# Performance work log

Hardware: AMD Instinct MI355X
Metric: run time of the kernel (lower is better)

## Reference

```python
import jax, jax.numpy as jnp
import numpy as np

B, S, D = 1, 4096, 2048
M = 4                  # compression rate
NC = S // M            # compressed slots
TOPK = 512
NH, C = 16, 64         # query heads, head dim
DC = 512               # query compression dim
NG, DG = 4, 512        # output projection groups, intermediate dim
CI, NHI = 64, 4        # indexer head dim, indexer heads
ROPE = 32              # partial rope dims (last ROPE of C)
EPS = 1e-6
NEG = -1e30


def _ln(x, w, b):
    mu = x.mean(-1, keepdims=True)
    var = ((x - mu) ** 2).mean(-1, keepdims=True)
    return (x - mu) * jax.lax.rsqrt(var + EPS) * w + b


def _rope(q, pos):
    # partial RoPE on the last ROPE dims of q [B,S,NH,C]; keys are NOT rotated (faithful)
    x_part, x_rope = q[..., :C - ROPE], q[..., C - ROPE:]
    x0, x1 = x_rope[..., 0::2], x_rope[..., 1::2]
    inv = 1.0 / (10000.0 ** (jnp.arange(0, ROPE, 2, dtype=jnp.float32) / ROPE))
    ang = pos[:, None].astype(jnp.float32) * inv[None]           # [S, ROPE/2]
    cos = jnp.cos(ang)[None, :, None, :]
    sin = jnp.sin(ang)[None, :, None, :]
    r = x0 * cos - x1 * sin
    i = x0 * sin + x1 * cos
    rot = jnp.stack([r, i], -1).reshape(x_rope.shape)
    return jnp.concatenate([x_part, rot], -1)


def reference(x, w_kv_a, w_kv_b, w_z_a, w_z_b, b_a, b_b, w_dq, w_iuq, w_w, w_k,
              w_uq, o_down, o_up, kvn_w, kvn_b, qn_w, qn_b, sink_logits):
    pos = jnp.arange(S)
    # ---- token-level compressor: windowed (2m-wide, m-stride) per-channel softmax ----
    c_a = (x @ w_kv_a).reshape(B, NC, M, C)
    c_b = (x @ w_kv_b).reshape(B, NC, M, C)
    z_a = (x @ w_z_a).reshape(B, NC, M, C)
    z_b = (x @ w_z_b).reshape(B, NC, M, C)
    prev_z = jnp.concatenate([jnp.full((B, 1, M, C), NEG, x.dtype), z_b[:, :-1]], 1)
    prev_c = jnp.concatenate([jnp.zeros((B, 1, M, C), x.dtype), c_b[:, :-1]], 1)
    logits = jnp.concatenate([prev_z + b_b, z_a + b_a], 2)        # [B,NC,2M,C]
    wts = jax.nn.softmax(logits, axis=2)
    compressed = (wts * jnp.concatenate([prev_c, c_a], 2)).sum(2)  # [B,NC,C]
    # ---- lightning indexer: relu multi-head scores + causal mask + top-k ----
    c_q = x @ w_dq                                                 # [B,S,DC]
    q_i = (c_q @ w_iuq).reshape(B, S, NHI, CI)
    hw = x @ w_w                                                   # [B,S,NHI]
    k_orig = x.reshape(B, NC, M, D).mean(2)
    k_proj = k_orig @ w_k                                          # [B,NC,CI]
    dot = jnp.einsum('bshc,bkc->bskh', q_i, k_proj)
    iscores = (jax.nn.relu(dot) * hw[:, :, None, :]).sum(-1)       # [B,S,NC]
    imask = jnp.arange(NC)[None, None, :] < pos[None, :, None]     # NC//S + 1 == 1
    iscores = jnp.where(imask, iscores, -jnp.inf)
    _, top_idx = jax.lax.top_k(iscores, TOPK)                      # [B,S,K]
    # ---- sparse attention over gathered compressed KV ----
    q = (c_q @ w_uq).reshape(B, S, NH, C)
    kc = _ln(compressed, kvn_w, kvn_b)
    q = _rope(_ln(q, qn_w, qn_b), pos)
    k_sel = kc[jnp.arange(B)[:, None, None], top_idx]              # [B,S,K,C]
    scores = jnp.einsum('bshc,bskc->bhsk', q, k_sel) / jnp.sqrt(jnp.float32(C))
    cmask = pos[None, None, :, None] < (top_idx[:, None, :, :] * M)
    scores = jnp.where(cmask, scores, -jnp.inf)
    e = jnp.exp(scores)
    denom = e.sum(-1, keepdims=True) + jnp.exp(sink_logits)[None, :, None, None]
    attn = e / denom                                               # sink-augmented softmax
    out = jnp.einsum('bhsk,bskc->bshc', attn, k_sel).reshape(B, S, NH * C)
    g = jnp.einsum('bsgd,gde->bsge', out.reshape(B, S, NG, (NH * C) // NG), o_down)
    return g.reshape(B, S, NG * DG) @ o_up


def setup_inputs() -> dict:
    key = jax.random.key(0)
    ks = jax.random.split(key, 20)
    lin = lambda k, fi, fo: jax.random.normal(k, (fi, fo), jnp.float32) / np.sqrt(fi)
    return {
        'x': jax.random.normal(ks[0], (B, S, D), jnp.float32),
        'w_kv_a': lin(ks[1], D, C), 'w_kv_b': lin(ks[2], D, C),
        'w_z_a': lin(ks[3], D, C), 'w_z_b': lin(ks[4], D, C),
        'b_a': 0.02 * jax.random.normal(ks[5], (M, C), jnp.float32),
        'b_b': 0.02 * jax.random.normal(ks[6], (M, C), jnp.float32),
        'w_dq': lin(ks[7], D, DC),
        'w_iuq': lin(ks[8], DC, CI * NHI),
        'w_w': lin(ks[9], D, NHI),
        'w_k': lin(ks[10], D, CI),
        'w_uq': lin(ks[11], DC, NH * C),
        'o_down': jax.random.normal(ks[12], (NG, (NH * C) // NG, DG), jnp.float32) / np.sqrt((NH * C) // NG),
        'o_up': lin(ks[13], NG * DG, D),
        'kvn_w': 1.0 + 0.02 * jax.random.normal(ks[14], (C,), jnp.float32),
        'kvn_b': 0.02 * jax.random.normal(ks[15], (C,), jnp.float32),
        'qn_w': 1.0 + 0.02 * jax.random.normal(ks[16], (C,), jnp.float32),
        'qn_b': 0.02 * jax.random.normal(ks[17], (C,), jnp.float32),
        'sink_logits': 0.02 * jax.random.normal(ks[18], (NH,), jnp.float32),
    }
```

## Files before the change

### kernel.cpp

```cpp
#include <hip/hip_runtime.h>
#include <math.h>

#define S_   4096
#define D_   2048
#define M_   4
#define NC_  1024
#define TOPK_ 512
#define NH_  16
#define C_   64
#define DC_  512
#define NG_  4
#define DG_  512
#define CI_  64
#define NHI_ 4
#define ROPE_ 32
#define EPS_ 1e-6f

typedef __attribute__((ext_vector_type(8))) short short8;
typedef __attribute__((ext_vector_type(4))) short short4v;
typedef __attribute__((ext_vector_type(4))) float floatx4;

__device__ inline unsigned short f2bf(float f) {
  unsigned u = __float_as_uint(f);
  u += 0x7fff + ((u >> 16) & 1);
  return (unsigned short)(u >> 16);
}
__device__ inline float bf2f(unsigned short h) {
  return __uint_as_float(((unsigned)h) << 16);
}

#define GLD16(src, dst) __builtin_amdgcn_global_load_lds( \
    (const __attribute__((address_space(1))) unsigned int*)(src), \
    (__attribute__((address_space(3))) unsigned int*)(dst), 16, 0, 0)

__device__ inline void xcd_remap(int& bx, int& by, int& bz) {
  int nx = gridDim.x, ny = gridDim.y;
  int flat = blockIdx.x + nx * (blockIdx.y + ny * blockIdx.z);
  int nwg = nx * ny * (int)gridDim.z;
  int swz = (flat & 7) * (nwg >> 3) + (flat >> 3);
  bx = swz % nx;
  int t = swz / nx;
  by = t % ny;
  bz = t / ny;
}

__global__ __launch_bounds__(256) void gemm_bf16_64(
    const unsigned short* __restrict__ A, const unsigned short* __restrict__ Bt,
    float* __restrict__ Cf, unsigned short* __restrict__ Cb,
    int K, int lda, int ldb, int ldc,
    long long Az, long long Bz, long long Cz) {
  int bx, by, zz;
  xcd_remap(bx, by, zz);
  A += (size_t)zz * Az;
  Bt += (size_t)zz * Bz;
  if (Cf) Cf += (size_t)zz * Cz;
  if (Cb) Cb += (size_t)zz * Cz;
  __shared__ unsigned short As[2 * 2 * 64 * 32];
  __shared__ unsigned short Bs[2 * 2 * 128 * 32];
  int tid = threadIdx.x;
  int bm = by * 64, bn = bx * 128;
  int lane = tid & 63, wid = tid >> 6;
  int wm = (wid & 1) * 32, wn = (wid >> 1) * 64;
  int qd = lane >> 4, m16 = lane & 15;

  floatx4 acc[2][4];
#pragma unroll
  for (int i = 0; i < 2; ++i)
#pragma unroll
    for (int j = 0; j < 4; ++j) acc[i][j] = (floatx4){0.f, 0.f, 0.f, 0.f};

  auto stage = [&](int buf, int kt) {
#pragma unroll
    for (int h = 0; h < 2; ++h) {
      {
        int rr = tid >> 2, ss = tid & 3;
        int gg = ss ^ ((rr >> 1) & 3);
        GLD16(A + (size_t)(bm + rr) * lda + kt + h * 32 + gg * 8,
              &As[(buf * 2 + h) * 2048 + tid * 8]);
      }
#pragma unroll
      for (int i = 0; i < 2; ++i) {
        int idx = tid + 256 * i;
        int rr = idx >> 2, ss = idx & 3;
        int gg = ss ^ ((rr >> 1) & 3);
        GLD16(Bt + (size_t)(bn + rr) * ldb + kt + h * 32 + gg * 8,
              &Bs[(buf * 2 + h) * 4096 + idx * 8]);
      }
    }
  };
  auto compute = [&](int buf) {
#pragma unroll
    for (int h = 0; h < 2; ++h) {
      const unsigned short* Ab = &As[(buf * 2 + h) * 2048];
      const unsigned short* Bb = &Bs[(buf * 2 + h) * 4096];
      short8 af[2], bfr[4];
#pragma unroll
      for (int mi = 0; mi < 2; ++mi) {
        int r = wm + mi * 16 + m16;
        int slot = qd ^ ((r >> 1) & 3);
        af[mi] = *(const short8*)&Ab[r * 32 + slot * 8];
      }
#pragma unroll
      for (int ni = 0; ni < 4; ++ni) {
        int r = wn + ni * 16 + m16;
        int slot = qd ^ ((r >> 1) & 3);
        bfr[ni] = *(const short8*)&Bb[r * 32 + slot * 8];
      }
#pragma unroll
      for (int mi = 0; mi < 2; ++mi)
#pragma unroll
        for (int ni = 0; ni < 4; ++ni)
          acc[mi][ni] = __builtin_amdgcn_mfma_f32_16x16x32_bf16(af[mi], bfr[ni], acc[mi][ni], 0, 0, 0);
    }
  };

  stage(0, 0);
  __syncthreads();
  int cur = 0;
  for (int kt = 64; kt < K; kt += 64) {
    stage(cur ^ 1, kt);
    compute(cur);
    __syncthreads();
    cur ^= 1;
  }
  compute(cur);

#pragma unroll
  for (int mi = 0; mi < 2; ++mi)
#pragma unroll
    for (int ni = 0; ni < 4; ++ni) {
      int col = bn + wn + ni * 16 + m16;
#pragma unroll
      for (int rg = 0; rg < 4; ++rg) {
        int row = bm + wm + mi * 16 + qd * 4 + rg;
        if (Cb)
          Cb[(size_t)row * ldc + col] = f2bf(acc[mi][ni][rg]);
        else
          Cf[(size_t)row * ldc + col] = acc[mi][ni][rg];
      }
    }
}

__global__ __launch_bounds__(256) void gemm_bf16_128(
    const unsigned short* __restrict__ A, const unsigned short* __restrict__ Bt,
    float* __restrict__ Cf, unsigned short* __restrict__ Cb,
    int K, int lda, int ldb, int ldc,
    long long Az, long long Bz, long long Cz) {
  int zz = blockIdx.z;
  A += (size_t)zz * Az;
  Bt += (size_t)zz * Bz;
  if (Cf) Cf += (size_t)zz * Cz;
  if (Cb) Cb += (size_t)zz * Cz;
  __shared__ unsigned short As[2 * 2 * 128 * 32];
  __shared__ unsigned short Bs[2 * 2 * 128 * 32];
  int tid = threadIdx.x;
  int bm = blockIdx.y * 128, bn = blockIdx.x * 128;
  int lane = tid & 63, wid = tid >> 6;
  int wm = (wid & 1) * 64, wn = (wid >> 1) * 64;
  int qd = lane >> 4, m16 = lane & 15;

  floatx4 acc[4][4];
#pragma unroll
  for (int i = 0; i < 4; ++i)
#pragma unroll
    for (int j = 0; j < 4; ++j) acc[i][j] = (floatx4){0.f, 0.f, 0.f, 0.f};

  auto stage = [&](int buf, int kt) {
#pragma unroll
    for (int h = 0; h < 2; ++h) {
#pragma unroll
      for (int i = 0; i < 2; ++i) {
        int idx = tid + 256 * i;
        int rr = idx >> 2, ss = idx & 3;
        int gg = ss ^ ((rr >> 1) & 3);
        GLD16(A + (size_t)(bm + rr) * lda + kt + h * 32 + gg * 8,
              &As[(buf * 2 + h) * 4096 + idx * 8]);
        GLD16(Bt + (size_t)(bn + rr) * ldb + kt + h * 32 + gg * 8,
              &Bs[(buf * 2 + h) * 4096 + idx * 8]);
      }
    }
  };
  auto compute = [&](int buf) {
#pragma unroll
    for (int h = 0; h < 2; ++h) {
      const unsigned short* Ab = &As[(buf * 2 + h) * 4096];
      const unsigned short* Bb = &Bs[(buf * 2 + h) * 4096];
      short8 af[4], bfr[4];
#pragma unroll
      for (int mi = 0; mi < 4; ++mi) {
        int r = wm + mi * 16 + m16;
        int slot = qd ^ ((r >> 1) & 3);
        af[mi] = *(const short8*)&Ab[r * 32 + slot * 8];
      }
#pragma unroll
      for (int ni = 0; ni < 4; ++ni) {
        int r = wn + ni * 16 + m16;
        int slot = qd ^ ((r >> 1) & 3);
        bfr[ni] = *(const short8*)&Bb[r * 32 + slot * 8];
      }
#pragma unroll
      for (int mi = 0; mi < 4; ++mi)
#pragma unroll
        for (int ni = 0; ni < 4; ++ni)
          acc[mi][ni] = __builtin_amdgcn_mfma_f32_16x16x32_bf16(af[mi], bfr[ni], acc[mi][ni], 0, 0, 0);
    }
  };

  stage(0, 0);
  __syncthreads();
  int cur = 0;
  for (int kt = 64; kt < K; kt += 64) {
    stage(cur ^ 1, kt);
    compute(cur);
    __syncthreads();
    cur ^= 1;
  }
  compute(cur);

#pragma unroll
  for (int mi = 0; mi < 4; ++mi)
#pragma unroll
    for (int ni = 0; ni < 4; ++ni) {
      int col = bn + wn + ni * 16 + m16;
#pragma unroll
      for (int rg = 0; rg < 4; ++rg) {
        int row = bm + wm + mi * 16 + qd * 4 + rg;
        if (Cb)
          Cb[(size_t)row * ldc + col] = f2bf(acc[mi][ni][rg]);
        else
          Cf[(size_t)row * ldc + col] = acc[mi][ni][rg];
      }
    }
}

__global__ __launch_bounds__(256) void gemm_bf16_split_64(
    const unsigned short* __restrict__ Ah, const unsigned short* __restrict__ Al,
    const unsigned short* __restrict__ Bh, const unsigned short* __restrict__ Bl,
    float* __restrict__ Cf, int K, int lda, int ldb, int ldc,
    long long Az, long long Bz, long long Cz) {
  int bx, by, zz;
  xcd_remap(bx, by, zz);
  Ah += (size_t)zz * Az; Al += (size_t)zz * Az;
  Bh += (size_t)zz * Bz; Bl += (size_t)zz * Bz;
  Cf += (size_t)zz * Cz;
  __shared__ unsigned short Ash[64 * 32];
  __shared__ unsigned short Asl[64 * 32];
  __shared__ unsigned short Bsh[128 * 32];
  __shared__ unsigned short Bsl[128 * 32];
  int tid = threadIdx.x;
  int bm = by * 64, bn = bx * 128;
  int lane = tid & 63, wid = tid >> 6;
  int wm = (wid & 1) * 32, wn = (wid >> 1) * 64;
  int qd = lane >> 4, m16 = lane & 15;

  floatx4 acc[2][4];
#pragma unroll
  for (int i = 0; i < 2; ++i)
#pragma unroll
    for (int j = 0; j < 4; ++j) acc[i][j] = (floatx4){0.f, 0.f, 0.f, 0.f};

  for (int k0 = 0; k0 < K; k0 += 32) {
    {
      int r = tid >> 2, sl = tid & 3;
      int g = sl ^ ((r >> 1) & 3);
      size_t aoff = (size_t)(bm + r) * lda + k0 + g * 8;
      GLD16(Ah + aoff, &Ash[tid * 8]);
      GLD16(Al + aoff, &Asl[tid * 8]);
    }
#pragma unroll
    for (int i = 0; i < 2; ++i) {
      int idx = tid + 256 * i;
      int r = idx >> 2, sl = idx & 3;
      int g = sl ^ ((r >> 1) & 3);
      size_t boff = (size_t)(bn + r) * ldb + k0 + g * 8;
      GLD16(Bh + boff, &Bsh[idx * 8]);
      GLD16(Bl + boff, &Bsl[idx * 8]);
    }
    __syncthreads();
    short8 afh[2], afl[2], bfh[4], bfl[4];
#pragma unroll
    for (int mi = 0; mi < 2; ++mi) {
      int r = wm + mi * 16 + m16;
      int slot = qd ^ ((r >> 1) & 3);
      afh[mi] = *(const short8*)&Ash[r * 32 + slot * 8];
      afl[mi] = *(const short8*)&Asl[r * 32 + slot * 8];
    }
#pragma unroll
    for (int ni = 0; ni < 4; ++ni) {
      int r = wn + ni * 16 + m16;
      int slot = qd ^ ((r >> 1) & 3);
      bfh[ni] = *(const short8*)&Bsh[r * 32 + slot * 8];
      bfl[ni] = *(const short8*)&Bsl[r * 32 + slot * 8];
    }
#pragma unroll
    for (int mi = 0; mi < 2; ++mi)
#pragma unroll
      for (int ni = 0; ni < 4; ++ni) {
        acc[mi][ni] = __builtin_amdgcn_mfma_f32_16x16x32_bf16(afh[mi], bfh[ni], acc[mi][ni], 0, 0, 0);
        acc[mi][ni] = __builtin_amdgcn_mfma_f32_16x16x32_bf16(afh[mi], bfl[ni], acc[mi][ni], 0, 0, 0);
        acc[mi][ni] = __builtin_amdgcn_mfma_f32_16x16x32_bf16(afl[mi], bfh[ni], acc[mi][ni], 0, 0, 0);
      }
    __syncthreads();
  }
#pragma unroll
  for (int mi = 0; mi < 2; ++mi)
#pragma unroll
    for (int ni = 0; ni < 4; ++ni) {
      int col = bn + wn + ni * 16 + m16;
#pragma unroll
      for (int rg = 0; rg < 4; ++rg) {
        int row = bm + wm + mi * 16 + qd * 4 + rg;
        Cf[(size_t)row * ldc + col] = acc[mi][ni][rg];
      }
    }
}

__global__ __launch_bounds__(256) void gemm_bf16_split_128(
    const unsigned short* __restrict__ Ah, const unsigned short* __restrict__ Al,
    const unsigned short* __restrict__ Bh, const unsigned short* __restrict__ Bl,
    float* __restrict__ Cf, int K, int lda, int ldb, int ldc,
    long long Az, long long Bz, long long Cz) {
  int bx, by, zz;
  xcd_remap(bx, by, zz);
  Ah += (size_t)zz * Az; Al += (size_t)zz * Az;
  Bh += (size_t)zz * Bz; Bl += (size_t)zz * Bz;
  Cf += (size_t)zz * Cz;
  __shared__ unsigned short Ash[2 * 128 * 32];
  __shared__ unsigned short Asl[2 * 128 * 32];
  __shared__ unsigned short Bsh[2 * 128 * 32];
  __shared__ unsigned short Bsl[2 * 128 * 32];
  int tid = threadIdx.x;
  int bm = by * 128, bn = bx * 128;
  int lane = tid & 63, wid = tid >> 6;
  int wm = (wid & 1) * 64, wn = (wid >> 1) * 64;
  int qd = lane >> 4, m16 = lane & 15;

  floatx4 acc[4][4];
#pragma unroll
  for (int i = 0; i < 4; ++i)
#pragma unroll
    for (int j = 0; j < 4; ++j) acc[i][j] = (floatx4){0.f, 0.f, 0.f, 0.f};

  auto stage = [&](int buf, int kt) {
#pragma unroll
    for (int i = 0; i < 2; ++i) {
      int idx = tid + 256 * i;
      int rr = idx >> 2, ss = idx & 3;
      int gg = ss ^ ((rr >> 1) & 3);
      size_t aoff = (size_t)(bm + rr) * lda + kt + gg * 8;
      size_t boff = (size_t)(bn + rr) * ldb + kt + gg * 8;
      GLD16(Ah + aoff, &Ash[buf * 4096 + idx * 8]);
      GLD16(Al + aoff, &Asl[buf * 4096 + idx * 8]);
      GLD16(Bh + boff, &Bsh[buf * 4096 + idx * 8]);
      GLD16(Bl + boff, &Bsl[buf * 4096 + idx * 8]);
    }
  };
  auto compute = [&](int buf) {
    const unsigned short* Ahb = &Ash[buf * 4096];
    const unsigned short* Alb = &Asl[buf * 4096];
    const unsigned short* Bhb = &Bsh[buf * 4096];
    const unsigned short* Blb = &Bsl[buf * 4096];
    short8 afh[4], afl[4], bfh[4], bfl[4];
#pragma unroll
    for (int mi = 0; mi < 4; ++mi) {
      int r = wm + mi * 16 + m16;
      int slot = qd ^ ((r >> 1) & 3);
      afh[mi] = *(const short8*)&Ahb[r * 32 + slot * 8];
      afl[mi] = *(const short8*)&Alb[r * 32 + slot * 8];
    }
#pragma unroll
    for (int ni = 0; ni < 4; ++ni) {
      int r = wn + ni * 16 + m16;
      int slot = qd ^ ((r >> 1) & 3);
      bfh[ni] = *(const short8*)&Bhb[r * 32 + slot * 8];
      bfl[ni] = *(const short8*)&Blb[r * 32 + slot * 8];
    }
#pragma unroll
    for (int mi = 0; mi < 4; ++mi)
#pragma unroll
      for (int ni = 0; ni < 4; ++ni) {
        acc[mi][ni] = __builtin_amdgcn_mfma_f32_16x16x32_bf16(afh[mi], bfh[ni], acc[mi][ni], 0, 0, 0);
        acc[mi][ni] = __builtin_amdgcn_mfma_f32_16x16x32_bf16(afh[mi], bfl[ni], acc[mi][ni], 0, 0, 0);
        acc[mi][ni] = __builtin_amdgcn_mfma_f32_16x16x32_bf16(afl[mi], bfh[ni], acc[mi][ni], 0, 0, 0);
      }
  };

  stage(0, 0);
  __syncthreads();
  int cur = 0;
  for (int kt = 32; kt < K; kt += 32) {
    stage(cur ^ 1, kt);
    compute(cur);
    __syncthreads();
    cur ^= 1;
  }
  compute(cur);

#pragma unroll
  for (int mi = 0; mi < 4; ++mi)
#pragma unroll
    for (int ni = 0; ni < 4; ++ni) {
      int col = bn + wn + ni * 16 + m16;
#pragma unroll
      for (int rg = 0; rg < 4; ++rg) {
        int row = bm + wm + mi * 16 + qd * 4 + rg;
        Cf[(size_t)row * ldc + col] = acc[mi][ni][rg];
      }
    }
}

__global__ void reduce_f32(const float* __restrict__ P, float* __restrict__ C, int n, int z) {
  int i = (blockIdx.x * 256 + threadIdx.x) * 4;
  if (i >= n) return;
  float4 a = *(const float4*)&P[i];
  for (int s = 1; s < z; ++s) {
    float4 b = *(const float4*)&P[(size_t)s * n + i];
    a.x += b.x; a.y += b.y; a.z += b.z; a.w += b.w;
  }
  *(float4*)&C[i] = a;
}

__global__ void reduce_cast_split(const float* __restrict__ P, unsigned short* __restrict__ hi,
                                  unsigned short* __restrict__ lo, int n, int z) {
  int i = (blockIdx.x * 256 + threadIdx.x) * 4;
  if (i >= n) return;
  float4 a = *(const float4*)&P[i];
  for (int s = 1; s < z; ++s) {
    float4 b = *(const float4*)&P[(size_t)s * n + i];
    a.x += b.x; a.y += b.y; a.z += b.z; a.w += b.w;
  }
  ushort4 h = make_ushort4(f2bf(a.x), f2bf(a.y), f2bf(a.z), f2bf(a.w));
  ushort4 l = make_ushort4(f2bf(a.x - bf2f(h.x)), f2bf(a.y - bf2f(h.y)),
                           f2bf(a.z - bf2f(h.z)), f2bf(a.w - bf2f(h.w)));
  *(ushort4*)&hi[i] = h;
  *(ushort4*)&lo[i] = l;
}

__global__ __launch_bounds__(256) void iscores_mfma(
    const unsigned short* __restrict__ Ah, const unsigned short* __restrict__ Al,
    const unsigned short* __restrict__ Bh, const unsigned short* __restrict__ Bl,
    const float* __restrict__ hw, float* __restrict__ isc) {
  int bm = blockIdx.y * 128, bn = blockIdx.x * 128;
  if (bn > (bm >> 2) + 30) return;
  __shared__ unsigned short Ash[128 * 32];
  __shared__ unsigned short Asl[128 * 32];
  __shared__ unsigned short Bsh[128 * 32];
  __shared__ unsigned short Bsl[128 * 32];
  int tid = threadIdx.x;
  int lane = tid & 63, wid = tid >> 6;
  int wm = (wid >> 1) * 64, wn = (wid & 1) * 64;
  int qd = lane >> 4, m16 = lane & 15;

  floatx4 acc[4][4];
#pragma unroll
  for (int i = 0; i < 4; ++i)
#pragma unroll
    for (int j = 0; j < 4; ++j) acc[i][j] = (floatx4){0.f, 0.f, 0.f, 0.f};

#pragma unroll
  for (int k0 = 0; k0 < 64; k0 += 32) {
#pragma unroll
    for (int i = 0; i < 2; ++i) {
      int idx = tid + 256 * i;
      int r = idx >> 2, s = idx & 3;
      int g = s ^ ((r >> 1) & 3);
      size_t aoff = (size_t)(bm + r) * 64 + k0 + g * 8;
      size_t boff = (size_t)(bn + r) * 64 + k0 + g * 8;
      GLD16(Ah + aoff, &Ash[idx * 8]);
      GLD16(Al + aoff, &Asl[idx * 8]);
      GLD16(Bh + boff, &Bsh[idx * 8]);
      GLD16(Bl + boff, &Bsl[idx * 8]);
    }
    __syncthreads();
    short8 afh[4], afl[4], bfh[4], bfl[4];
#pragma unroll
    for (int mi = 0; mi < 4; ++mi) {
      int r = wm + mi * 16 + m16;
      int slot = qd ^ ((r >> 1) & 3);
      afh[mi] = *(const short8*)&Ash[r * 32 + slot * 8];
      afl[mi] = *(const short8*)&Asl[r * 32 + slot * 8];
    }
#pragma unroll
    for (int ni = 0; ni < 4; ++ni) {
      int r = wn + ni * 16 + m16;
      int slot = qd ^ ((r >> 1) & 3);
      bfh[ni] = *(const short8*)&Bsh[r * 32 + slot * 8];
      bfl[ni] = *(const short8*)&Bsl[r * 32 + slot * 8];
    }
#pragma unroll
    for (int mi = 0; mi < 4; ++mi)
#pragma unroll
      for (int ni = 0; ni < 4; ++ni) {
        acc[mi][ni] = __builtin_amdgcn_mfma_f32_16x16x32_bf16(afh[mi], bfh[ni], acc[mi][ni], 0, 0, 0);
        acc[mi][ni] = __builtin_amdgcn_mfma_f32_16x16x32_bf16(afh[mi], bfl[ni], acc[mi][ni], 0, 0, 0);
        acc[mi][ni] = __builtin_amdgcn_mfma_f32_16x16x32_bf16(afl[mi], bfh[ni], acc[mi][ni], 0, 0, 0);
      }
    __syncthreads();
  }
#pragma unroll
  for (int mi = 0; mi < 4; ++mi) {
    int tok = ((bm + wm + mi * 16) >> 2) + qd;
    float4 hwv = *(const float4*)&hw[tok * 4];
#pragma unroll
    for (int ni = 0; ni < 4; ++ni) {
      floatx4 a = acc[mi][ni];
      float v = fmaxf(a[0], 0.f) * hwv.x + fmaxf(a[1], 0.f) * hwv.y +
                fmaxf(a[2], 0.f) * hwv.z + fmaxf(a[3], 0.f) * hwv.w;
      int col = bn + wn + ni * 16 + m16;
      isc[(size_t)tok * NC_ + col] = (col < tok) ? v : -__builtin_inff();
    }
  }
}

#define BM 64
#define BN 64
#define BK 16
#define KSL_ 16
#define KSLICE_ 128
__global__ __launch_bounds__(256) void gemm_f32_splitk(
    const float* __restrict__ A, const float* __restrict__ B,
    float* __restrict__ P, int lda, int ldb) {
  __shared__ float As[BK][BM + 4];
  __shared__ float Bs[BK][BN + 4];
  int tid = threadIdx.x;
  int bm = blockIdx.y * BM;
  int kbase = blockIdx.x * KSLICE_;
  int tr = tid >> 4;
  int tc = tid & 15;
  float acc[4][4] = {{0.f}};
  for (int k0 = kbase; k0 < kbase + KSLICE_; k0 += BK) {
    int ac = tid & 15;
    int ar0 = tid >> 4;
#pragma unroll
    for (int i = 0; i < 4; ++i) {
      int r = ar0 + 16 * i;
      As[ac][r] = A[(size_t)(bm + r) * lda + k0 + ac];
    }
    int bc = tid & 63;
    int br0 = tid >> 6;
#pragma unroll
    for (int i = 0; i < 4; ++i) {
      int r = br0 + 4 * i;
      Bs[r][bc] = B[(size_t)(k0 + r) * ldb + bc];
    }
    __syncthreads();
#pragma unroll
    for (int kk = 0; kk < BK; ++kk) {
      float4 av = *(const float4*)&As[kk][tr * 4];
      float4 bv = *(const float4*)&Bs[kk][tc * 4];
      float a[4] = {av.x, av.y, av.z, av.w};
      float b[4] = {bv.x, bv.y, bv.z, bv.w};
#pragma unroll
      for (int i = 0; i < 4; ++i)
#pragma unroll
        for (int j = 0; j < 4; ++j) acc[i][j] += a[i] * b[j];
    }
    __syncthreads();
  }
  float* Pb = P + (size_t)blockIdx.x * (NC_ * CI_);
#pragma unroll
  for (int i = 0; i < 4; ++i) {
    float4 v = make_float4(acc[i][0], acc[i][1], acc[i][2], acc[i][3]);
    *(float4*)&Pb[(size_t)(bm + tr * 4 + i) * CI_ + tc * 4] = v;
  }
}

__global__ void reduce_splitk(const float* __restrict__ P, float* __restrict__ C) {
  int i = blockIdx.x * 256 + threadIdx.x;
  if (i >= NC_ * CI_) return;
  float a = 0.f;
#pragma unroll
  for (int s = 0; s < KSL_; ++s) a += P[(size_t)s * (NC_ * CI_) + i];
  C[i] = a;
}

__global__ void cast_bf16(const float* __restrict__ in, unsigned short* __restrict__ out, int n) {
  int i = (blockIdx.x * 256 + threadIdx.x) * 4;
  if (i >= n) return;
  float4 v = *(const float4*)&in[i];
  ushort4 o = make_ushort4(f2bf(v.x), f2bf(v.y), f2bf(v.z), f2bf(v.w));
  *(ushort4*)&out[i] = o;
}

__global__ void cast_split(const float* __restrict__ in, unsigned short* __restrict__ hi,
                           unsigned short* __restrict__ lo, int n) {
  int i = (blockIdx.x * 256 + threadIdx.x) * 4;
  if (i >= n) return;
  float4 v = *(const float4*)&in[i];
  ushort4 h = make_ushort4(f2bf(v.x), f2bf(v.y), f2bf(v.z), f2bf(v.w));
  ushort4 l = make_ushort4(f2bf(v.x - bf2f(h.x)), f2bf(v.y - bf2f(h.y)),
                           f2bf(v.z - bf2f(h.z)), f2bf(v.w - bf2f(h.w)));
  *(ushort4*)&hi[i] = h;
  *(ushort4*)&lo[i] = l;
}

__device__ inline float wave_sum64(float v) {
#pragma unroll
  for (int off = 32; off > 0; off >>= 1) v += __shfl_xor(v, off, 64);
  return v;
}

__global__ __launch_bounds__(512) void cast_split_hw_mean(
    const float* __restrict__ x, unsigned short* __restrict__ hi,
    unsigned short* __restrict__ lo, const float* __restrict__ ww,
    float* __restrict__ hw, float* __restrict__ ko) {
  int j = blockIdx.x, tid = threadIdx.x;
  int d0 = tid * 4;
  const float* wr = ww + d0 * 4;
  float4 v[4];
  float a[4][4];
#pragma unroll
  for (int m = 0; m < 4; ++m) {
    size_t i = (size_t)(j * 4 + m) * D_ + d0;
    v[m] = *(const float4*)&x[i];
    ushort4 h = make_ushort4(f2bf(v[m].x), f2bf(v[m].y), f2bf(v[m].z), f2bf(v[m].w));
    ushort4 l = make_ushort4(f2bf(v[m].x - bf2f(h.x)), f2bf(v[m].y - bf2f(h.y)),
                             f2bf(v[m].z - bf2f(h.z)), f2bf(v[m].w - bf2f(h.w)));
    *(ushort4*)&hi[i] = h;
    *(ushort4*)&lo[i] = l;
    a[m][0] = v[m].x * wr[0] + v[m].y * wr[4] + v[m].z * wr[8]  + v[m].w * wr[12];
    a[m][1] = v[m].x * wr[1] + v[m].y * wr[5] + v[m].z * wr[9]  + v[m].w * wr[13];
    a[m][2] = v[m].x * wr[2] + v[m].y * wr[6] + v[m].z * wr[10] + v[m].w * wr[14];
    a[m][3] = v[m].x * wr[3] + v[m].y * wr[7] + v[m].z * wr[11] + v[m].w * wr[15];
  }
  float4 s4;
  s4.x = 0.25f * (v[0].x + v[1].x + v[2].x + v[3].x);
  s4.y = 0.25f * (v[0].y + v[1].y + v[2].y + v[3].y);
  s4.z = 0.25f * (v[0].z + v[1].z + v[2].z + v[3].z);
  s4.w = 0.25f * (v[0].w + v[1].w + v[2].w + v[3].w);
  *(float4*)&ko[(size_t)j * D_ + d0] = s4;
#pragma unroll
  for (int m = 0; m < 4; ++m)
#pragma unroll
    for (int h2 = 0; h2 < 4; ++h2) a[m][h2] = wave_sum64(a[m][h2]);
  __shared__ float red[8][16];
  int wid = tid >> 6, lane = tid & 63;
  if (lane == 0) {
#pragma unroll
    for (int m = 0; m < 4; ++m)
#pragma unroll
      for (int h2 = 0; h2 < 4; ++h2) red[wid][m * 4 + h2] = a[m][h2];
  }
  __syncthreads();
  if (tid < 16) {
    float acc = 0.f;
#pragma unroll
    for (int w2 = 0; w2 < 8; ++w2) acc += red[w2][tid];
    hw[(size_t)(j * 4 + (tid >> 2)) * 4 + (tid & 3)] = acc;
  }
}

__global__ __launch_bounds__(256) void transpose_cast(
    const float* __restrict__ in, unsigned short* __restrict__ out, int K, int N,
    long long inz, long long outz) {
  in += (size_t)blockIdx.z * inz;
  out += (size_t)blockIdx.z * outz;
  __shared__ float t[32][33];
  int k0 = blockIdx.x * 32, n0 = blockIdx.y * 32;
  int tx = threadIdx.x & 31, ty = threadIdx.x >> 5;
#pragma unroll
  for (int i = 0; i < 4; ++i)
    t[ty * 4 + i][tx] = in[(size_t)(k0 + ty * 4 + i) * N + n0 + tx];
  __syncthreads();
#pragma unroll
  for (int i = 0; i < 4; ++i)
    out[(size_t)(n0 + ty * 4 + i) * K + k0 + tx] = f2bf(t[tx][ty * 4 + i]);
}

__global__ __launch_bounds__(256) void transpose_cast_split(
    const float* __restrict__ in, unsigned short* __restrict__ outh,
    unsigned short* __restrict__ outl, int K, int N) {
  __shared__ float t[32][33];
  int k0 = blockIdx.x * 32, n0 = blockIdx.y * 32;
  int tx = threadIdx.x & 31, ty = threadIdx.x >> 5;
#pragma unroll
  for (int i = 0; i < 4; ++i)
    t[ty * 4 + i][tx] = in[(size_t)(k0 + ty * 4 + i) * N + n0 + tx];
  __syncthreads();
#pragma unroll
  for (int i = 0; i < 4; ++i) {
    float v = t[tx][ty * 4 + i];
    unsigned short h = f2bf(v);
    outh[(size_t)(n0 + ty * 4 + i) * K + k0 + tx] = h;
    outl[(size_t)(n0 + ty * 4 + i) * K + k0 + tx] = f2bf(v - bf2f(h));
  }
}

__global__ void gate_kernel(const float* __restrict__ c4,
                            const float* __restrict__ ba, const float* __restrict__ bb,
                            float* __restrict__ comp) {
  int i = blockIdx.x * 256 + threadIdx.x;
  if (i >= NC_ * C_) return;
  int j = i >> 6, c = i & 63;
  float lg[8], vv[8];
#pragma unroll
  for (int m = 0; m < 4; ++m) {
    if (j == 0) {
      lg[m] = -1e30f + bb[m * C_ + c];
      vv[m] = 0.f;
    } else {
      int row = (j - 1) * 4 + m;
      lg[m] = c4[(size_t)row * 256 + 192 + c] + bb[m * C_ + c];
      vv[m] = c4[(size_t)row * 256 + 64 + c];
    }
    int row2 = j * 4 + m;
    lg[4 + m] = c4[(size_t)row2 * 256 + 128 + c] + ba[m * C_ + c];
    vv[4 + m] = c4[(size_t)row2 * 256 + 0 + c];
  }
  float mx = lg[0];
#pragma unroll
  for (int t = 1; t < 8; ++t) mx = fmaxf(mx, lg[t]);
  float se = 0.f, acc = 0.f;
#pragma unroll
  for (int t = 0; t < 8; ++t) {
    float e = expf(lg[t] - mx);
    se += e;
    acc += e * vv[t];
  }
  comp[i] = acc / se;
}

__global__ void ln_kc_kernel(const float* __restrict__ in, const float* __restrict__ w,
                             const float* __restrict__ b, unsigned short* __restrict__ kcb,
                             unsigned short* __restrict__ kcbT) {
  int row = blockIdx.x * 4 + (threadIdx.x >> 6);
  int c = threadIdx.x & 63;
  float v = in[(size_t)row * C_ + c];
  float mu = wave_sum64(v) * (1.f / 64.f);
  float d = v - mu;
  float var = wave_sum64(d * d) * (1.f / 64.f);
  float y = d * (1.f / sqrtf(var + EPS_)) * w[c] + b[c];
  unsigned short h = f2bf(y);
  kcb[(size_t)row * C_ + c] = h;
  kcbT[(size_t)c * NC_ + row] = h;
}

__global__ void ln_rope_q_kernel(const float* __restrict__ quq, const float* __restrict__ w,
                                 const float* __restrict__ b, unsigned short* __restrict__ qb) {
  int row = blockIdx.x * 4 + (threadIdx.x >> 6);
  int s = row >> 4;
  int c = threadIdx.x & 63;
  float v = quq[(size_t)row * C_ + c];
  float mu = wave_sum64(v) * (1.f / 64.f);
  float d = v - mu;
  float var = wave_sum64(d * d) * (1.f / 64.f);
  float y = d * (1.f / sqrtf(var + EPS_)) * w[c] + b[c];
  float outv;
  float partner = __shfl_xor(y, 1, 64);
  if (c < C_ - ROPE_) {
    outv = y;
  } else {
    int p = (c - (C_ - ROPE_)) >> 1;
    float inv = powf(10000.f, -(2.f * (float)p) / (float)ROPE_);
    float ang = (float)s * inv;
    float cs = cosf(ang), sn = sinf(ang);
    if ((c & 1) == 0)
      outv = y * cs - partner * sn;
    else
      outv = partner * sn + y * cs;
  }
  qb[(size_t)row * C_ + c] = f2bf(outv * 0.125f);
}

#define MINF_ 0x007FFFFFu
__global__ __launch_bounds__(256) void topk_select_kernel(
    const float* __restrict__ isc, unsigned* __restrict__ sel) {
  __shared__ unsigned mv[NC_];
  __shared__ unsigned bins[256];
  __shared__ unsigned wsum[4];
  __shared__ unsigned sB, sR;
  __shared__ unsigned selw[32];
  int s = blockIdx.x;
  int tid = threadIdx.x;
  int w = tid >> 6, lane = tid & 63;
  if (tid < 32) selw[tid] = 0u;
  for (int i = tid; i < NC_; i += 256) {
    if (i < s) {
      unsigned u = __float_as_uint(isc[(size_t)s * NC_ + i]);
      mv[i] = (u & 0x80000000u) ? ~u : (u | 0x80000000u);
    } else {
      mv[i] = MINF_;
    }
  }
  __syncthreads();
  unsigned K_rem = TOPK_;
  unsigned prefix = 0u;
  for (int lvl = 0; lvl < 4; ++lvl) {
    int shift = 24 - 8 * lvl;
    unsigned pm = (lvl == 0) ? 0u : (0xFFFFFFFFu << (32 - 8 * lvl));
    bins[tid] = 0u;
    __syncthreads();
    for (int i = tid; i < NC_; i += 256) {
      unsigned m = mv[i];
      if ((m & pm) == prefix) atomicAdd(&bins[(m >> shift) & 0xFFu], 1u);
    }
    __syncthreads();
    unsigned v = bins[tid];
    unsigned p = v;
#pragma unroll
    for (int off = 1; off < 64; off <<= 1) {
      unsigned n = __shfl_up(p, (unsigned)off, 64);
      if (lane >= off) p += n;
    }
    if (lane == 63) wsum[w] = p;
    __syncthreads();
    unsigned T = 0, woff = 0;
#pragma unroll
    for (int i = 0; i < 4; ++i) {
      unsigned x_ = wsum[i];
      T += x_;
      if (i < w) woff += x_;
    }
    p += woff;
    unsigned gt = T - p;
    if (gt < K_rem && K_rem <= gt + v) { sB = (unsigned)tid; sR = K_rem - gt; }
    __syncthreads();
    prefix |= (sB << shift);
    K_rem = sR;
  }
  unsigned vstar = prefix;
  unsigned eq = 0;
#pragma unroll
  for (int j = 0; j < 4; ++j) eq += (mv[4 * tid + j] == vstar);
  unsigned rp = eq;
#pragma unroll
  for (int off = 1; off < 64; off <<= 1) {
    unsigned n = __shfl_up(rp, (unsigned)off, 64);
    if (lane >= off) rp += n;
  }
  if (lane == 63) wsum[w] = rp;
  __syncthreads();
  unsigned woff2 = 0;
#pragma unroll
  for (int i = 0; i < 4; ++i)
    if (i < w) woff2 += wsum[i];
  unsigned rank0 = rp + woff2 - eq;
  unsigned local = 0, bits = 0;
#pragma unroll
  for (int j = 0; j < 4; ++j) {
    unsigned m = mv[4 * tid + j];
    bool sb = (m > vstar) || (m == vstar && (rank0 + local) < K_rem);
    local += (m == vstar);
    if (sb) bits |= (1u << ((4 * tid + j) & 31));
  }
  if (bits) atomicOr(&selw[tid >> 3], bits);
  __syncthreads();
  if (tid < 32) sel[(size_t)s * 32 + tid] = selw[tid];
}

#define TS_ 8
__global__ __launch_bounds__(256) void attn_mfma_kernel(
    const unsigned short* __restrict__ qb, const unsigned short* __restrict__ kcb,
    const unsigned short* __restrict__ kcbT, const unsigned* __restrict__ sel,
    const float* __restrict__ sink, unsigned short* __restrict__ out) {
  __shared__ unsigned short kc_s[64 * 72];
  __shared__ unsigned short kct_s[64 * 72];
  __shared__ unsigned short p_s[128 * 72];
  __shared__ unsigned selw[TS_][32];
  __shared__ float dls[4][2][16];
  int tid = threadIdx.x;
  int s0 = blockIdx.x * TS_;
  int lane = tid & 63, w = tid >> 6;
  int qd = lane >> 4, m16 = lane & 15;

  for (int i = tid; i < TS_ * 32; i += 256)
    selw[i >> 5][i & 31] = sel[(size_t)(s0 + (i >> 5)) * 32 + (i & 31)];

  short8 qf[2][2];
#pragma unroll
  for (int tk = 0; tk < 2; ++tk)
#pragma unroll
    for (int ks = 0; ks < 2; ++ks)
      qf[tk][ks] = *(const short8*)&qb[(size_t)(s0 + 2 * w + tk) * 1024 + m16 * 64 + ks * 32 + qd * 8];

  floatx4 of[2][4];
#pragma unroll
  for (int i = 0; i < 2; ++i)
#pragma unroll
    for (int j = 0; j < 4; ++j) of[i][j] = (floatx4){0.f, 0.f, 0.f, 0.f};
  float dsum[2] = {0.f, 0.f};

  int ub = max(511, s0 + TS_ - 2);
  int ct_start = max(0, (s0 + 4) >> 8);
  int ct_end = min(16, (ub >> 6) + 1);

  for (int ct = ct_start; ct < ct_end; ++ct) {
    int c0 = ct * 64;
    __syncthreads();
    {
      int r = tid >> 2, cc = (tid & 3) * 16;
      *(short8*)&kc_s[r * 72 + cc]      = *(const short8*)&kcb[(size_t)(c0 + r) * 64 + cc];
      *(short8*)&kc_s[r * 72 + cc + 8]  = *(const short8*)&kcb[(size_t)(c0 + r) * 64 + cc + 8];
      *(short8*)&kct_s[r * 72 + cc]     = *(const short8*)&kcbT[(size_t)r * NC_ + c0 + cc];
      *(short8*)&kct_s[r * 72 + cc + 8] = *(const short8*)&kcbT[(size_t)r * NC_ + c0 + cc + 8];
    }
    __syncthreads();
#pragma unroll
    for (int mc = 0; mc < 4; ++mc) {
      short8 a0 = *(const short8*)&kc_s[(mc * 16 + m16) * 72 + qd * 8];
      short8 a1 = *(const short8*)&kc_s[(mc * 16 + m16) * 72 + 32 + qd * 8];
#pragma unroll
      for (int nt = 0; nt < 2; ++nt) {
        floatx4 sc = (floatx4){0.f, 0.f, 0.f, 0.f};
        sc = __builtin_amdgcn_mfma_f32_16x16x32_bf16(a0, qf[nt][0], sc, 0, 0, 0);
        sc = __builtin_amdgcn_mfma_f32_16x16x32_bf16(a1, qf[nt][1], sc, 0, 0, 0);
        int tokL = 2 * w + nt;
        int sG = s0 + tokL;
        short4v pv;
#pragma unroll
        for (int rg = 0; rg < 4; ++rg) {
          int cG = c0 + mc * 16 + qd * 4 + rg;
          bool ok = (((selw[tokL][cG >> 5] >> (cG & 31)) & 1u) != 0u) && (sG < cG * 4);
          float e = ok ? __expf(sc[rg]) : 0.f;
          dsum[nt] += e;
          pv[rg] = (short)f2bf(e);
        }
        *(short4v*)&p_s[(tokL * 16 + m16) * 72 + mc * 16 + qd * 4] = pv;
      }
    }
#pragma unroll
    for (int ks = 0; ks < 2; ++ks) {
      short8 pa0 = *(const short8*)&p_s[((2 * w + 0) * 16 + m16) * 72 + ks * 32 + qd * 8];
      short8 pa1 = *(const short8*)&p_s[((2 * w + 1) * 16 + m16) * 72 + ks * 32 + qd * 8];
#pragma unroll
      for (int nt = 0; nt < 4; ++nt) {
        short8 bv = *(const short8*)&kct_s[(nt * 16 + m16) * 72 + ks * 32 + qd * 8];
        of[0][nt] = __builtin_amdgcn_mfma_f32_16x16x32_bf16(pa0, bv, of[0][nt], 0, 0, 0);
        of[1][nt] = __builtin_amdgcn_mfma_f32_16x16x32_bf16(pa1, bv, of[1][nt], 0, 0, 0);
      }
    }
  }
#pragma unroll
  for (int nt = 0; nt < 2; ++nt) {
    dsum[nt] += __shfl_xor(dsum[nt], 16, 64);
    dsum[nt] += __shfl_xor(dsum[nt], 32, 64);
  }
  if (lane < 16) {
    float sk = __expf(sink[lane]);
    dls[w][0][lane] = dsum[0] + sk;
    dls[w][1][lane] = dsum[1] + sk;
  }
  __syncthreads();
#pragma unroll
  for (int tk = 0; tk < 2; ++tk)
#pragma unroll
    for (int nt = 0; nt < 4; ++nt) {
      floatx4 o = of[tk][nt];
#pragma unroll
      for (int rg = 0; rg < 4; ++rg) {
        int head = qd * 4 + rg;
        float dn = dls[w][tk][head];
        out[(size_t)(s0 + 2 * w + tk) * 1024 + head * 64 + nt * 16 + m16] = f2bf(o[rg] / dn);
      }
    }
}

#define OFF_QUQ    0u
#define OFF_Q      4194304u
#define OFF_XH     8388608u
#define OFF_XL     12582912u
#define OFF_PART   16777216u
#define OFF_KO     18874368u
#define OFF_C4     20971520u
#define OFF_CQF    22020096u
#define OFF_WTB    24117248u
#define OFF_CQH    25165824u
#define OFF_CQL    26214400u
#define OFF_WPACKT 27262976u
#define OFF_WDQTH  27525120u
#define OFF_WDQTL  28049408u
#define OFF_WIUQTH 28573696u
#define OFF_WIUQTL 28639232u
#define OFF_WUQT   28704768u
#define OFF_ODB    28966912u
#define OFF_OUPT   29229056u
#define OFF_HW     31326208u
#define OFF_COMP   31342592u
#define OFF_KC     31408128u
#define OFF_KPR    31473664u

extern "C" void kernel_launch(void* const* d_in, const int* in_sizes, int n_in,
                              void* d_out, int out_size, void* d_ws, size_t ws_size,
                              hipStream_t stream) {
  const float* x      = (const float*)d_in[0];
  const float* w_kv_a = (const float*)d_in[1];
  const float* w_kv_b = (const float*)d_in[2];
  const float* w_z_a  = (const float*)d_in[3];
  const float* w_z_b  = (const float*)d_in[4];
  const float* b_a    = (const float*)d_in[5];
  const float* b_b    = (const float*)d_in[6];
  const float* w_dq   = (const float*)d_in[7];
  const float* w_iuq  = (const float*)d_in[8];
  const float* w_w    = (const float*)d_in[9];
  const float* w_k    = (const float*)d_in[10];
  const float* w_uq   = (const float*)d_in[11];
  const float* o_down = (const float*)d_in[12];
  const float* o_up   = (const float*)d_in[13];
  const float* kvn_w  = (const float*)d_in[14];
  const float* kvn_b  = (const float*)d_in[15];
  const float* qn_w   = (const float*)d_in[16];
  const float* qn_b   = (const float*)d_in[17];
  const float* sink   = (const float*)d_in[18];
  float* out = (float*)d_out;
  float* ws = (float*)d_ws;

  float* quq   = ws + OFF_QUQ;
  float* isc   = ws + OFF_QUQ;
  unsigned short* qb = (unsigned short*)(ws + OFF_Q);
  unsigned short* xh = (unsigned short*)(ws + OFF_XH);
  unsigned short* xl = (unsigned short*)(ws + OFF_XL);
  unsigned* sel = (unsigned*)(ws + OFF_XL);
  float* part  = ws + OFF_PART;
  float* k_or  = ws + OFF_KO;
  unsigned short* attnb = (unsigned short*)(ws + OFF_KO);
  float* c4    = ws + OFF_C4;
  unsigned short* qih = (unsigned short*)(ws + OFF_CQF);
  unsigned short* qil = qih + S_ * NHI_ * CI_;
  unsigned short* kph = qil + S_ * NHI_ * CI_;
  unsigned short* kpl = kph + NC_ * CI_;
  unsigned short* wtb = (unsigned short*)(ws + OFF_WTB);
  unsigned short* cqh = (unsigned short*)(ws + OFF_CQH);
  unsigned short* cql = (unsigned short*)(ws + OFF_CQL);
  unsigned short* wpackT = (unsigned short*)(ws + OFF_WPACKT);
  unsigned short* wdqTh  = (unsigned short*)(ws + OFF_WDQTH);
  unsigned short* wdqTl  = (unsigned short*)(ws + OFF_WDQTL);
  unsigned short* wiuqTh = (unsigned short*)(ws + OFF_WIUQTH);
  unsigned short* wiuqTl = (unsigned short*)(ws + OFF_WIUQTL);
  unsigned short* wuqT   = (unsigned short*)(ws + OFF_WUQT);
  unsigned short* odb    = (unsigned short*)(ws + OFF_ODB);
  unsigned short* oupT   = (unsigned short*)(ws + OFF_OUPT);
  float* hw    = ws + OFF_HW;
  float* comp  = ws + OFF_COMP;
  unsigned short* kcb  = (unsigned short*)(ws + OFF_KC);
  unsigned short* kcbT = kcb + NC_ * C_;
  float* k_pr  = ws + OFF_KPR;

  dim3 blk(256);

  cast_split_hw_mean<<<NC_, dim3(512), 0, stream>>>(x, xh, xl, w_w, hw, k_or);
  transpose_cast<<<dim3(64, 2), blk, 0, stream>>>(w_kv_a, wpackT + 0 * 64 * 2048, D_, C_, 0, 0);
  transpose_cast<<<dim3(64, 2), blk, 0, stream>>>(w_kv_b, wpackT + 1 * 64 * 2048, D_, C_, 0, 0);
  transpose_cast<<<dim3(64, 2), blk, 0, stream>>>(w_z_a,  wpackT + 2 * 64 * 2048, D_, C_, 0, 0);
  transpose_cast<<<dim3(64, 2), blk, 0, stream>>>(w_z_b,  wpackT + 3 * 64 * 2048, D_, C_, 0, 0);
  transpose_cast_split<<<dim3(64, 16), blk, 0, stream>>>(w_dq, wdqTh, wdqTl, D_, DC_);
  transpose_cast_split<<<dim3(16, 8), blk, 0, stream>>>(w_iuq, wiuqTh, wiuqTl, DC_, NHI_ * CI_);
  transpose_cast<<<dim3(16, 32), blk, 0, stream>>>(w_uq, wuqT, DC_, NH_ * C_, 0, 0);
  cast_bf16<<<512, blk, 0, stream>>>(o_down, odb, NG_ * 256 * DG_);
  transpose_cast<<<dim3(64, 64), blk, 0, stream>>>(o_up, oupT, NG_ * DG_, D_, 0, 0);

  gemm_bf16_64<<<dim3(2, 32, 4), blk, 0, stream>>>(
      oupT, odb, nullptr, wtb, DG_, D_, DG_, NG_ * 256,
      (long long)DG_, (long long)256 * DG_, 256LL);

  gemm_f32_splitk<<<dim3(KSL_, 16), blk, 0, stream>>>(k_or, w_k, part, D_, CI_);
  reduce_splitk<<<256, blk, 0, stream>>>(part, k_pr);

  gemm_bf16_split_128<<<dim3(4, 32, 4), blk, 0, stream>>>(xh, xl, wdqTh, wdqTl, ws,
                                                          512, D_, D_, DC_, 512, 512, (long long)S_ * DC_);
  reduce_cast_split<<<2048, blk, 0, stream>>>(ws, cqh, cql, S_ * DC_, 4);
  gemm_bf16_64<<<dim3(2, 64, 4), blk, 0, stream>>>(xh, wpackT, part, nullptr,
                                                   512, D_, D_, 256, 512, 512, (long long)S_ * 256);
  reduce_f32<<<1024, blk, 0, stream>>>(part, c4, S_ * 256, 4);
  gemm_bf16_split_64<<<dim3(2, 64, 4), blk, 0, stream>>>(cqh, cql, wiuqTh, wiuqTl, part,
                                                         128, DC_, DC_, 256, 128, 128, (long long)S_ * 256);
  reduce_cast_split<<<1024, blk, 0, stream>>>(part, qih, qil, S_ * 256, 4);
  gemm_bf16_64<<<dim3(8, 64, 1), blk, 0, stream>>>(cqh, wuqT, quq, nullptr,
                                                   DC_, DC_, DC_, NH_ * C_, 0, 0, 0);

  gate_kernel<<<256, blk, 0, stream>>>(c4, b_a, b_b, comp);
  ln_kc_kernel<<<256, blk, 0, stream>>>(comp, kvn_w, kvn_b, kcb, kcbT);

  ln_rope_q_kernel<<<16384, blk, 0, stream>>>(quq, qn_w, qn_b, qb);

  cast_split<<<64, blk, 0, stream>>>(k_pr, kph, kpl, NC_ * CI_);
  iscores_mfma<<<dim3(8, 128), blk, 0, stream>>>(qih, qil, kph, kpl, hw, isc);
  topk_select_kernel<<<S_, blk, 0, stream>>>(isc, sel);

  attn_mfma_kernel<<<S_ / TS_, blk, 0, stream>>>(qb, kcb, kcbT, sel, sink, attnb);

  gemm_bf16_128<<<dim3(16, 32, 1), blk, 0, stream>>>(attnb, wtb, out, nullptr,
                                                     NG_ * 256, NH_ * C_, NG_ * 256, D_, 0, 0, 0);
}
```

Baseline: 411.2 us.

## Read attention K tiles from global, precompute RoPE table, remap GEMM blocks per XCD

```diff
diff --git a/kernel.cpp b/kernel.cpp
--- a/kernel.cpp
+++ b/kernel.cpp
@@ -146,7 +146,8 @@
     float* __restrict__ Cf, unsigned short* __restrict__ Cb,
     int K, int lda, int ldb, int ldc,
     long long Az, long long Bz, long long Cz) {
-  int zz = blockIdx.z;
+  int bx, by, zz;
+  xcd_remap(bx, by, zz);
   A += (size_t)zz * Az;
   Bt += (size_t)zz * Bz;
   if (Cf) Cf += (size_t)zz * Cz;
@@ -154,7 +155,7 @@
   __shared__ unsigned short As[2 * 2 * 128 * 32];
   __shared__ unsigned short Bs[2 * 2 * 128 * 32];
   int tid = threadIdx.x;
-  int bm = blockIdx.y * 128, bn = blockIdx.x * 128;
+  int bm = by * 128, bn = bx * 128;
   int lane = tid & 63, wid = tid >> 6;
   int wm = (wid & 1) * 64, wn = (wid >> 1) * 64;
   int qd = lane >> 4, m16 = lane & 15;
@@ -735,8 +736,19 @@
   kcbT[(size_t)c * NC_ + row] = h;
 }
 
+__global__ void rope_table_kernel(float* __restrict__ rt) {
+  int i = blockIdx.x * 256 + threadIdx.x;
+  if (i >= S_ * 16) return;
+  int s = i >> 4, p = i & 15;
+  float inv = powf(10000.f, -(2.f * (float)p) / (float)ROPE_);
+  float ang = (float)s * inv;
+  rt[i * 2] = cosf(ang);
+  rt[i * 2 + 1] = sinf(ang);
+}
+
 __global__ void ln_rope_q_kernel(const float* __restrict__ quq, const float* __restrict__ w,
-                                 const float* __restrict__ b, unsigned short* __restrict__ qb) {
+                                 const float* __restrict__ b, const float* __restrict__ rt,
+                                 unsigned short* __restrict__ qb) {
   int row = blockIdx.x * 4 + (threadIdx.x >> 6);
   int s = row >> 4;
   int c = threadIdx.x & 63;
@@ -751,9 +763,8 @@
     outv = y;
   } else {
     int p = (c - (C_ - ROPE_)) >> 1;
-    float inv = powf(10000.f, -(2.f * (float)p) / (float)ROPE_);
-    float ang = (float)s * inv;
-    float cs = cosf(ang), sn = sinf(ang);
+    float cs = rt[(s * 16 + p) * 2];
+    float sn = rt[(s * 16 + p) * 2 + 1];
     if ((c & 1) == 0)
       outv = y * cs - partner * sn;
     else
@@ -853,18 +864,14 @@
     const unsigned short* __restrict__ qb, const unsigned short* __restrict__ kcb,
     const unsigned short* __restrict__ kcbT, const unsigned* __restrict__ sel,
     const float* __restrict__ sink, unsigned short* __restrict__ out) {
-  __shared__ unsigned short kc_s[64 * 72];
-  __shared__ unsigned short kct_s[64 * 72];
   __shared__ unsigned short p_s[128 * 72];
   __shared__ unsigned selw[TS_][32];
-  __shared__ float dls[4][2][16];
   int tid = threadIdx.x;
   int s0 = blockIdx.x * TS_;
   int lane = tid & 63, w = tid >> 6;
   int qd = lane >> 4, m16 = lane & 15;
 
-  for (int i = tid; i < TS_ * 32; i += 256)
-    selw[i >> 5][i & 31] = sel[(size_t)(s0 + (i >> 5)) * 32 + (i & 31)];
+  selw[tid >> 5][tid & 31] = sel[(size_t)(s0 + (tid >> 5)) * 32 + (tid & 31)];
 
   short8 qf[2][2];
 #pragma unroll
@@ -886,19 +893,10 @@
 
   for (int ct = ct_start; ct < ct_end; ++ct) {
     int c0 = ct * 64;
-    __syncthreads();
-    {
-      int r = tid >> 2, cc = (tid & 3) * 16;
-      *(short8*)&kc_s[r * 72 + cc]      = *(const short8*)&kcb[(size_t)(c0 + r) * 64 + cc];
-      *(short8*)&kc_s[r * 72 + cc + 8]  = *(const short8*)&kcb[(size_t)(c0 + r) * 64 + cc + 8];
-      *(short8*)&kct_s[r * 72 + cc]     = *(const short8*)&kcbT[(size_t)r * NC_ + c0 + cc];
-      *(short8*)&kct_s[r * 72 + cc + 8] = *(const short8*)&kcbT[(size_t)r * NC_ + c0 + cc + 8];
-    }
-    __syncthreads();
 #pragma unroll
     for (int mc = 0; mc < 4; ++mc) {
-      short8 a0 = *(const short8*)&kc_s[(mc * 16 + m16) * 72 + qd * 8];
-      short8 a1 = *(const short8*)&kc_s[(mc * 16 + m16) * 72 + 32 + qd * 8];
+      short8 a0 = *(const short8*)&kcb[(size_t)(c0 + mc * 16 + m16) * 64 + qd * 8];
+      short8 a1 = *(const short8*)&kcb[(size_t)(c0 + mc * 16 + m16) * 64 + 32 + qd * 8];
 #pragma unroll
       for (int nt = 0; nt < 2; ++nt) {
         floatx4 sc = (floatx4){0.f, 0.f, 0.f, 0.f};
@@ -924,7 +922,7 @@
       short8 pa1 = *(const short8*)&p_s[((2 * w + 1) * 16 + m16) * 72 + ks * 32 + qd * 8];
 #pragma unroll
       for (int nt = 0; nt < 4; ++nt) {
-        short8 bv = *(const short8*)&kct_s[(nt * 16 + m16) * 72 + ks * 32 + qd * 8];
+        short8 bv = *(const short8*)&kcbT[(size_t)(nt * 16 + m16) * NC_ + c0 + ks * 32 + qd * 8];
         of[0][nt] = __builtin_amdgcn_mfma_f32_16x16x32_bf16(pa0, bv, of[0][nt], 0, 0, 0);
         of[1][nt] = __builtin_amdgcn_mfma_f32_16x16x32_bf16(pa1, bv, of[1][nt], 0, 0, 0);
       }
@@ -935,12 +933,6 @@
     dsum[nt] += __shfl_xor(dsum[nt], 16, 64);
     dsum[nt] += __shfl_xor(dsum[nt], 32, 64);
   }
-  if (lane < 16) {
-    float sk = __expf(sink[lane]);
-    dls[w][0][lane] = dsum[0] + sk;
-    dls[w][1][lane] = dsum[1] + sk;
-  }
-  __syncthreads();
 #pragma unroll
   for (int tk = 0; tk < 2; ++tk)
 #pragma unroll
@@ -949,7 +941,7 @@
 #pragma unroll
       for (int rg = 0; rg < 4; ++rg) {
         int head = qd * 4 + rg;
-        float dn = dls[w][tk][head];
+        float dn = __shfl(dsum[tk], head, 64) + __expf(sink[head]);
         out[(size_t)(s0 + 2 * w + tk) * 1024 + head * 64 + nt * 16 + m16] = f2bf(o[rg] / dn);
       }
     }
@@ -963,6 +955,7 @@
 #define OFF_KO     18874368u
 #define OFF_C4     20971520u
 #define OFF_CQF    22020096u
+#define OFF_RT     23134208u
 #define OFF_WTB    24117248u
 #define OFF_CQH    25165824u
 #define OFF_CQL    26214400u
@@ -1018,6 +1011,7 @@
   unsigned short* qil = qih + S_ * NHI_ * CI_;
   unsigned short* kph = qil + S_ * NHI_ * CI_;
   unsigned short* kpl = kph + NC_ * CI_;
+  float* rt    = ws + OFF_RT;
   unsigned short* wtb = (unsigned short*)(ws + OFF_WTB);
   unsigned short* cqh = (unsigned short*)(ws + OFF_CQH);
   unsigned short* cql = (unsigned short*)(ws + OFF_CQL);
@@ -1038,6 +1032,7 @@
   dim3 blk(256);
 
   cast_split_hw_mean<<<NC_, dim3(512), 0, stream>>>(x, xh, xl, w_w, hw, k_or);
+  rope_table_kernel<<<256, blk, 0, stream>>>(rt);
   transpose_cast<<<dim3(64, 2), blk, 0, stream>>>(w_kv_a, wpackT + 0 * 64 * 2048, D_, C_, 0, 0);
   transpose_cast<<<dim3(64, 2), blk, 0, stream>>>(w_kv_b, wpackT + 1 * 64 * 2048, D_, C_, 0, 0);
   transpose_cast<<<dim3(64, 2), blk, 0, stream>>>(w_z_a,  wpackT + 2 * 64 * 2048, D_, C_, 0, 0);
@@ -1070,7 +1065,7 @@
   gate_kernel<<<256, blk, 0, stream>>>(c4, b_a, b_b, comp);
   ln_kc_kernel<<<256, blk, 0, stream>>>(comp, kvn_w, kvn_b, kcb, kcbT);
 
-  ln_rope_q_kernel<<<16384, blk, 0, stream>>>(quq, qn_w, qn_b, qb);
+  ln_rope_q_kernel<<<16384, blk, 0, stream>>>(quq, qn_w, qn_b, rt, qb);
 
   cast_split<<<64, blk, 0, stream>>>(k_pr, kph, kpl, NC_ * CI_);
   iscores_mfma<<<dim3(8, 128), blk, 0, stream>>>(qih, qil, kph, kpl, hw, isc);
```

Measured after the change: 410.9 us. Within noise of the previous version (-0.1%).
